# Kernel tuning notes

Measured on AMD Instinct MI355X. Metric: run time of the kernel, lower is better.

The kernel has to match this reference:

```python
import jax, jax.numpy as jnp
import numpy as np

N_NODES = 100000
N_EDGES = 600000
D = 128  # input_dim == output_dim (required by index_add into zeros_like(x) + residual)
EPS = 1e-5


def _linear_params(key, d_in, d_out):
    kw, kb = jax.random.split(key)
    bound = 1.0 / np.sqrt(d_in)
    w = jax.random.uniform(kw, (d_in, d_out), minval=-bound, maxval=bound, dtype=jnp.float32)
    b = jax.random.uniform(kb, (d_out,), minval=-bound, maxval=bound, dtype=jnp.float32)
    return w, b


def setup_inputs() -> dict:
    key = jax.random.key(0)
    ks = jax.random.split(key, 6)
    x = jax.random.normal(ks[0], (N_NODES, D), dtype=jnp.float32)
    edge_index = jax.random.randint(ks[1], (2, N_EDGES), 0, N_NODES, dtype=jnp.int32)
    w_m1, b_m1 = _linear_params(ks[2], 2 * D, D)
    w_m2, b_m2 = _linear_params(ks[3], D, D)
    w_u1, b_u1 = _linear_params(ks[4], 2 * D, D)
    w_u2, b_u2 = _linear_params(ks[5], D, D)
    gamma = jnp.ones((D,), dtype=jnp.float32)
    beta = jnp.zeros((D,), dtype=jnp.float32)
    return {
        "x": x, "edge_index": edge_index,
        "w_m1": w_m1, "b_m1": b_m1, "w_m2": w_m2, "b_m2": b_m2,
        "w_u1": w_u1, "b_u1": b_u1, "w_u2": w_u2, "b_u2": b_u2,
        "gamma": gamma, "beta": beta,
    }


def _layernorm(h, gamma, beta):
    mu = jnp.mean(h, axis=-1, keepdims=True)
    var = jnp.mean(jnp.square(h - mu), axis=-1, keepdims=True)
    return (h - mu) * jax.lax.rsqrt(var + EPS) * gamma + beta


def reference(x, edge_index, w_m1, b_m1, w_m2, b_m2, w_u1, b_u1, w_u2, b_u2, gamma, beta):
    row, col = edge_index[0], edge_index[1]
    # message MLP on concat of gathered endpoints: [E, 2D] -> [E, D]
    m_in = jnp.concatenate([x[row], x[col]], axis=-1)
    m = jax.nn.relu(m_in @ w_m1 + b_m1) @ w_m2 + b_m2
    # scatter-add messages to destination nodes (index_add along dim 0 with col)
    agg = jax.ops.segment_sum(m, col, num_segments=x.shape[0])
    # update MLP on [N, 2D] -> [N, D]
    u_in = jnp.concatenate([x, agg], axis=-1)
    h = jax.nn.relu(u_in @ w_u1 + b_u1) @ w_u2 + b_u2
    return _layernorm(h, gamma, beta) + x
```

## Files before the change

### kernel.cpp

```cpp
#include <hip/hip_runtime.h>
#include <hip/hip_bf16.h>
#include <stdint.h>

#define N_NODES 100000
#define N_EDGES 600000
#define D 128
#define EPS 1e-5f
#define SCAN_BS 512
#define ROW_MASK 0x1FFFF

#define PREP_BLOCKS 321
#define HIST_BLOCKS 2344
#define XF_BLOCKS   782

typedef __attribute__((ext_vector_type(8))) short short8;
typedef __attribute__((ext_vector_type(16))) float floatx16;


__device__ __forceinline__ uint32_t pack_bf16_rne(float lo, float hi) {
    uint32_t ul = __builtin_bit_cast(uint32_t, lo);
    uint32_t uh = __builtin_bit_cast(uint32_t, hi);
    ul += 0x7fffu + ((ul >> 16) & 1u);
    uh += 0x7fffu + ((uh >> 16) & 1u);
    return (ul >> 16) | (uh & 0xffff0000u);
}

__device__ __forceinline__ unsigned short f32_to_bf16_rne(float f) {
    uint32_t u = __builtin_bit_cast(uint32_t, f);
    u += 0x7fffu + ((u >> 16) & 1u);
    return (unsigned short)(u >> 16);
}

__device__ __forceinline__ float bflo(uint32_t a) { return __builtin_bit_cast(float, a << 16); }
__device__ __forceinline__ float bfhi(uint32_t a) { return __builtin_bit_cast(float, a & 0xffff0000u); }

__global__ void prep_hist(const float* __restrict__ w_m1, const float* __restrict__ w_u1,
                          const float* __restrict__ w_u2, const float* __restrict__ w_m2,
                          const float* __restrict__ b_m2,
                          unsigned short* __restrict__ wm1f, unsigned short* __restrict__ wu1tf,
                          unsigned short* __restrict__ wu2f, unsigned short* __restrict__ wcf,
                          float* __restrict__ vb,
                          const int* __restrict__ col, int* __restrict__ count) {
    if (blockIdx.x >= PREP_BLOCKS) {
        int e = (blockIdx.x - PREP_BLOCKS) * 256 + threadIdx.x;
        if (e < N_EDGES) atomicAdd(&count[col[e]], 1);
        return;
    }
    int idx = blockIdx.x * 256 + threadIdx.x;
    if (idx < 32768) {
        int j = idx & 7, lane = (idx >> 3) & 63, t = (idx >> 9) & 3, s = idx >> 11;
        int kk = s * 16 + ((lane >> 5) << 3) + j;
        wm1f[idx] = f32_to_bf16_rne(w_m1[kk * 128 + t * 32 + (lane & 31)]);
    } else if (idx < 49152) {
        int ii = idx - 32768;
        int j = ii & 7, lane = (ii >> 3) & 63, t = (ii >> 9) & 3, s = ii >> 11;
        int kk = s * 16 + ((lane >> 5) << 3) + j;
        wu1tf[ii] = f32_to_bf16_rne(w_u1[kk * 128 + t * 32 + (lane & 31)]);
    } else if (idx < 65536) {
        int ii = idx - 49152;
        int j = ii & 7, lane = (ii >> 3) & 63, t = (ii >> 9) & 3, s = ii >> 11;
        int kk = s * 16 + ((lane >> 5) << 3) + j;
        wu2f[ii] = f32_to_bf16_rne(w_u2[kk * 128 + t * 32 + (lane & 31)]);
    } else if (idx < 81920) {
        int ii = idx - 65536;
        int j = ii & 7, lane = (ii >> 3) & 63, t = (ii >> 9) & 3, s = ii >> 11;
        int kk = s * 16 + ((lane >> 5) << 3) + j;
        int nn = t * 32 + (lane & 31);
        float acc = 0.0f;
        for (int q = 0; q < 128; ++q)
            acc += w_m2[kk * 128 + q] * w_u1[(128 + q) * 128 + nn];
        wcf[ii] = f32_to_bf16_rne(acc);
    } else if (idx < 82048) {
        int nn = idx - 81920;
        float acc = 0.0f;
        for (int q = 0; q < 128; ++q)
            acc += b_m2[q] * w_u1[(128 + q) * 128 + nn];
        vb[nn] = acc;
    }
}

__global__ void scan_one(const int* __restrict__ count, int* __restrict__ base,
                         int* __restrict__ cursor, int* __restrict__ gcur) {
    __shared__ int tmp[SCAN_BS];
    __shared__ int bbase;
    int g = blockIdx.x * SCAN_BS + threadIdx.x;
    int v = (g < N_NODES) ? count[g] : 0;
    tmp[threadIdx.x] = v;
    __syncthreads();
    int acc = v;
#pragma unroll
    for (int off = 1; off < SCAN_BS; off <<= 1) {
        int add = (threadIdx.x >= off) ? tmp[threadIdx.x - off] : 0;
        __syncthreads();
        acc += add;
        tmp[threadIdx.x] = acc;
        __syncthreads();
    }
    if (threadIdx.x == SCAN_BS - 1) bbase = atomicAdd(gcur, acc);
    __syncthreads();
    if (g < N_NODES) {
        int b = bbase + acc - v;
        base[g] = b;
        cursor[g] = b;
    }
}

__launch_bounds__(256, 4)
__global__ void xform_scatter(const float* __restrict__ x, const short8* __restrict__ w1f,
                              const float* __restrict__ b1, unsigned short* __restrict__ xtb,
                              const int* __restrict__ row, const int* __restrict__ col,
                              int* __restrict__ cursor, int* __restrict__ srow) {
    if (blockIdx.x >= XF_BLOCKS) {
        int e = (blockIdx.x - XF_BLOCKS) * 256 + threadIdx.x;
        if (e < N_EDGES) {
            int c = col[e];
            int p = atomicAdd(&cursor[c], 1);
            srow[p] = row[e] | ((c & 31) << 17);
        }
        return;
    }

    __shared__ __align__(16) short h1[4][32 * 136];
    const int wave = threadIdx.x >> 6;
    const int lane = threadIdx.x & 63;
    const int l31  = lane & 31;
    const int half = lane >> 5;
    short* hl = h1[wave];

    const int nbase = (blockIdx.x * 4 + wave) * 32;
    const int n = min(nbase + l31, N_NODES - 1);
    const float* px = x + (size_t)n * D + half * 8;

    union { short8 v; uint32_t u[4]; } fa[8];
#pragma unroll
    for (int s = 0; s < 8; ++s) {
        const int off = s * 16;
        float4 a0 = *(const float4*)(px + off);
        float4 a1 = *(const float4*)(px + off + 4);
        fa[s].u[0] = pack_bf16_rne(a0.x, a0.y); fa[s].u[1] = pack_bf16_rne(a0.z, a0.w);
        fa[s].u[2] = pack_bf16_rne(a1.x, a1.y); fa[s].u[3] = pack_bf16_rne(a1.z, a1.w);
    }

#pragma unroll
    for (int p = 0; p < 2; ++p) {
        floatx16 acc[4];
#pragma unroll
        for (int t = 0; t < 4; ++t) acc[t] = (floatx16)0.0f;
#pragma unroll
        for (int s = 0; s < 8; ++s) {
#pragma unroll
            for (int t = 0; t < 4; ++t) {
                short8 wf = w1f[((p * 8 + s) * 4 + t) * 64 + lane];
                acc[t] = __builtin_amdgcn_mfma_f32_32x32x16_bf16(fa[s].v, wf, acc[t], 0, 0, 0);
            }
        }
#pragma unroll
        for (int t = 0; t < 4; ++t) {
            float bias = p ? b1[t * 32 + l31] : 0.0f;
#pragma unroll
            for (int r = 0; r < 16; ++r) {
                int m = (r & 3) + 8 * (r >> 2) + 4 * half;
                hl[m * 136 + t * 32 + l31] = (short)f32_to_bf16_rne(acc[t][r] + bias);
            }
        }
#pragma unroll
        for (int it = 0; it < 8; ++it) {
            int off = it * 512 + lane * 8;
            int r2 = off >> 7;
            int c2 = off & 127;
            if (nbase + r2 < N_NODES) {
                short8 v = *(const short8*)(hl + r2 * 136 + c2);
                *(short8*)(xtb + (size_t)(nbase + r2) * 256 + p * 128 + c2) = v;
            }
        }
    }
}

__launch_bounds__(256, 4)
__global__ void upd_kernel(const float* __restrict__ x, const uint32_t* __restrict__ xtb32,
                           const int* __restrict__ srowpk,
                           const int* __restrict__ base, const int* __restrict__ count,
                           const short8* __restrict__ wu1tf, const short8* __restrict__ wcf,
                           const short8* __restrict__ wu2f,
                           const float* __restrict__ b_u1, const float* __restrict__ vb,
                           const float* __restrict__ b_u2,
                           const float* __restrict__ gamma, const float* __restrict__ beta,
                           float* __restrict__ out) {
    __shared__ __align__(16) short h1[4][32 * 136];
    const int wave = threadIdx.x >> 6;
    const int lane = threadIdx.x & 63;
    const int l31  = lane & 31;
    const int half = lane >> 5;
    short* hl = h1[wave];
    uint32_t* accu = (uint32_t*)hl;

    const int nbase = (blockIdx.x * 4 + wave) * 32;
    const int nc = min(nbase + l31, N_NODES - 1);

    const int b_l = base[nc];
    const int c_l = count[nc];
    const int ebeg = __shfl(b_l, 0);
    const int eend = __shfl(b_l, 31) + __shfl(c_l, 31);
    const float dgv = (float)c_l;

#pragma unroll
    for (int i = 0; i < 32; ++i) accu[i * 64 + lane] = 0;

    {
        float s_lo = 0.0f, s_hi = 0.0f;
        int curnib = -1;
        for (int t0 = ebeg; t0 < eend; t0 += 64) {
            const int nb = min(64, eend - t0);
            int pk = (lane < nb) ? srowpk[t0 + lane] : 0;
            for (int d = 0; d < nb; d += 4) {
                int p0 = __shfl(pk, d);
                int p1 = __shfl(pk, min(d + 1, nb - 1));
                int p2 = __shfl(pk, min(d + 2, nb - 1));
                int p3 = __shfl(pk, min(d + 3, nb - 1));
                int r0 = p0 & ROW_MASK, n0 = p0 >> 17;
                int r1 = p1 & ROW_MASK, n1 = p1 >> 17;
                int r2 = p2 & ROW_MASK, n2 = p2 >> 17;
                int r3 = p3 & ROW_MASK, n3 = p3 >> 17;
                uint32_t a0 = xtb32[(size_t)r0 * 128 + lane];
                uint32_t b0 = xtb32[(size_t)(nbase + n0) * 128 + 64 + lane];
                uint32_t a1 = xtb32[(size_t)r1 * 128 + lane];
                uint32_t b1v = xtb32[(size_t)(nbase + n1) * 128 + 64 + lane];
                uint32_t a2 = xtb32[(size_t)r2 * 128 + lane];
                uint32_t b2v = xtb32[(size_t)(nbase + n2) * 128 + 64 + lane];
                uint32_t a3 = xtb32[(size_t)r3 * 128 + lane];
                uint32_t b3v = xtb32[(size_t)(nbase + n3) * 128 + 64 + lane];

                {
                    float vlo = fmaxf(bflo(a0) + bflo(b0), 0.0f);
                    float vhi = fmaxf(bfhi(a0) + bfhi(b0), 0.0f);
                    if (n0 != curnib) {
                        if (curnib >= 0) accu[curnib * 64 + lane] = pack_bf16_rne(s_lo, s_hi);
                        curnib = n0; s_lo = vlo; s_hi = vhi;
                    } else { s_lo += vlo; s_hi += vhi; }
                }
                if (d + 1 < nb) {
                    float vlo = fmaxf(bflo(a1) + bflo(b1v), 0.0f);
                    float vhi = fmaxf(bfhi(a1) + bfhi(b1v), 0.0f);
                    if (n1 != curnib) {
                        accu[curnib * 64 + lane] = pack_bf16_rne(s_lo, s_hi);
                        curnib = n1; s_lo = vlo; s_hi = vhi;
                    } else { s_lo += vlo; s_hi += vhi; }
                }
                if (d + 2 < nb) {
                    float vlo = fmaxf(bflo(a2) + bflo(b2v), 0.0f);
                    float vhi = fmaxf(bfhi(a2) + bfhi(b2v), 0.0f);
                    if (n2 != curnib) {
                        accu[curnib * 64 + lane] = pack_bf16_rne(s_lo, s_hi);
                        curnib = n2; s_lo = vlo; s_hi = vhi;
                    } else { s_lo += vlo; s_hi += vhi; }
                }
                if (d + 3 < nb) {
                    float vlo = fmaxf(bflo(a3) + bflo(b3v), 0.0f);
                    float vhi = fmaxf(bfhi(a3) + bfhi(b3v), 0.0f);
                    if (n3 != curnib) {
                        accu[curnib * 64 + lane] = pack_bf16_rne(s_lo, s_hi);
                        curnib = n3; s_lo = vlo; s_hi = vhi;
                    } else { s_lo += vlo; s_hi += vhi; }
                }
            }
        }
        if (curnib >= 0) accu[curnib * 64 + lane] = pack_bf16_rne(s_lo, s_hi);
    }

    const float* px = x + (size_t)nc * D + half * 8;

    floatx16 acc[4];
#pragma unroll
    for (int t = 0; t < 4; ++t) acc[t] = (floatx16)0.0f;

#pragma unroll
    for (int s = 0; s < 16; ++s) {
        union { short8 v; uint32_t u[4]; } fa;
        const short8* bf;
        if (s < 8) {
            const int off = s * 16;
            float4 a0 = *(const float4*)(px + off);
            float4 a1 = *(const float4*)(px + off + 4);
            fa.u[0] = pack_bf16_rne(a0.x, a0.y); fa.u[1] = pack_bf16_rne(a0.z, a0.w);
            fa.u[2] = pack_bf16_rne(a1.x, a1.y); fa.u[3] = pack_bf16_rne(a1.z, a1.w);
            bf = wu1tf + (s * 4) * 64;
        } else {
            fa.v = *(const short8*)((const short*)accu + l31 * 128 + (s - 8) * 16 + half * 8);
            bf = wcf + ((s - 8) * 4) * 64;
        }
#pragma unroll
        for (int t = 0; t < 4; ++t) {
            short8 wf = bf[t * 64 + lane];
            acc[t] = __builtin_amdgcn_mfma_f32_32x32x16_bf16(fa.v, wf, acc[t], 0, 0, 0);
        }
    }

    float bu1[4], vbt[4];
#pragma unroll
    for (int t = 0; t < 4; ++t) {
        bu1[t] = b_u1[t * 32 + l31];
        vbt[t] = vb[t * 32 + l31];
    }

#pragma unroll
    for (int r = 0; r < 16; ++r) {
        int m = (r & 3) + 8 * (r >> 2) + 4 * half;
        float dg = __shfl(dgv, m, 32);
#pragma unroll
        for (int t = 0; t < 4; ++t) {
            float v = fmaxf(acc[t][r] + bu1[t] + dg * vbt[t], 0.0f);
            hl[m * 136 + t * 32 + l31] = (short)f32_to_bf16_rne(v);
        }
    }

    floatx16 acc2[4];
#pragma unroll
    for (int t = 0; t < 4; ++t) acc2[t] = (floatx16)0.0f;

#pragma unroll
    for (int s = 0; s < 8; ++s) {
        short8 af = *(const short8*)(hl + l31 * 136 + s * 16 + half * 8);
#pragma unroll
        for (int t = 0; t < 4; ++t) {
            short8 wf = wu2f[(s * 4 + t) * 64 + lane];
            acc2[t] = __builtin_amdgcn_mfma_f32_32x32x16_bf16(af, wf, acc2[t], 0, 0, 0);
        }
    }

    float g4[4], be4[4], bias2[4];
#pragma unroll
    for (int t = 0; t < 4; ++t) {
        g4[t]    = gamma[t * 32 + l31];
        be4[t]   = beta[t * 32 + l31];
        bias2[t] = b_u2[t * 32 + l31];
    }

    float* hf = (float*)hl;
#pragma unroll
    for (int p = 0; p < 2; ++p) {
#pragma unroll
        for (int rr = 0; rr < 8; ++rr) {
            int r = p * 8 + rr;
            float hv[4];
            float s1 = 0.0f, s2 = 0.0f;
#pragma unroll
            for (int t = 0; t < 4; ++t) {
                hv[t] = acc2[t][r] + bias2[t];
                s1 += hv[t];
                s2 += hv[t] * hv[t];
            }
#pragma unroll
            for (int mask = 1; mask < 32; mask <<= 1) {
                s1 += __shfl_xor(s1, mask);
                s2 += __shfl_xor(s2, mask);
            }
            float mean = s1 * (1.0f / 128.0f);
            float var  = s2 * (1.0f / 128.0f) - mean * mean;
            float rs   = rsqrtf(var + EPS);
            int m = (r & 3) + 8 * (r >> 2) + 4 * half;
            int mrow = m - 16 * p;
#pragma unroll
            for (int t = 0; t < 4; ++t)
                hf[mrow * 132 + t * 32 + l31] = (hv[t] - mean) * rs * g4[t] + be4[t];
        }
#pragma unroll
        for (int it = 0; it < 8; ++it) {
            int q = it * 64 + lane;
            int r2 = q >> 5;
            int c4 = q & 31;
            int node = nbase + 16 * p + r2;
            if (node < N_NODES) {
                float4 v = *(const float4*)(hf + r2 * 132 + c4 * 4);
                float4 xr = *(const float4*)(x + (size_t)node * D + c4 * 4);
                v.x += xr.x; v.y += xr.y; v.z += xr.z; v.w += xr.w;
                *(float4*)(out + (size_t)node * D + c4 * 4) = v;
            }
        }
    }
}

extern "C" void kernel_launch(void* const* d_in, const int* in_sizes, int n_in,
                              void* d_out, int out_size, void* d_ws, size_t ws_size,
                              hipStream_t stream) {
    const float* x     = (const float*)d_in[0];
    const int*   edge  = (const int*)d_in[1];
    const float* w_m1  = (const float*)d_in[2];
    const float* b_m1  = (const float*)d_in[3];
    const float* w_m2  = (const float*)d_in[4];
    const float* b_m2  = (const float*)d_in[5];
    const float* w_u1  = (const float*)d_in[6];
    const float* b_u1  = (const float*)d_in[7];
    const float* w_u2  = (const float*)d_in[8];
    const float* b_u2  = (const float*)d_in[9];
    const float* gamma = (const float*)d_in[10];
    const float* beta  = (const float*)d_in[11];
    float* out = (float*)d_out;

    char* ws = (char*)d_ws;
    size_t off = 0;
    auto alloc = [&](size_t bytes) { void* p = ws + off; off = (off + bytes + 15) & ~(size_t)15; return p; };

    unsigned short* xtb   = (unsigned short*)alloc((size_t)N_NODES * 256 * 2);
    unsigned short* wm1f  = (unsigned short*)alloc(256 * 128 * 2);
    unsigned short* wu1tf = (unsigned short*)alloc(128 * 128 * 2);
    unsigned short* wcf   = (unsigned short*)alloc(128 * 128 * 2);
    unsigned short* wu2f  = (unsigned short*)alloc(128 * 128 * 2);
    float* vb    = (float*)alloc(128 * 4);
    int* count   = (int*)alloc((size_t)N_NODES * 4 + 16);
    int* gcur    = count + N_NODES;
    int* base    = (int*)alloc((size_t)N_NODES * 4);
    int* cursor  = (int*)alloc((size_t)N_NODES * 4);
    int* srow    = (int*)alloc((size_t)N_EDGES * 4);

    const int* rowi = edge;
    const int* coli = edge + N_EDGES;
    const int NB = (N_NODES + SCAN_BS - 1) / SCAN_BS;

    (void)hipMemsetAsync(count, 0, (size_t)N_NODES * 4 + 16, stream);

    prep_hist<<<PREP_BLOCKS + HIST_BLOCKS, 256, 0, stream>>>(
        w_m1, w_u1, w_u2, w_m2, b_m2, wm1f, wu1tf, wu2f, wcf, vb, coli, count);

    scan_one<<<NB, SCAN_BS, 0, stream>>>(count, base, cursor, gcur);

    xform_scatter<<<XF_BLOCKS + HIST_BLOCKS, 256, 0, stream>>>(
        x, (const short8*)wm1f, b_m1, xtb, rowi, coli, cursor, srow);

    upd_kernel<<<(N_NODES + 127) / 128, 256, 0, stream>>>(
        x, (const uint32_t*)xtb, srow, base, count,
        (const short8*)wu1tf, (const short8*)wcf, (const short8*)wu2f,
        b_u1, vb, b_u2, gamma, beta, out);
}
```

Measured before the change: 269.5 us.

## Record histogram ranks to drop scatter atomics, use one-wave blocks, widen gather batch

The histogram pass now saves each edge's atomic rank. The scatter pass computes its slot as base[col]+rank, so it no longer needs a second pass of atomics or a cursor array. The transform and update kernels are relaunched with single-wave 64-thread blocks (one 32-node tile per block), and the tail-bound guards are removed because 100000 divides evenly into 32-node tiles. The update kernel's edge gather now issues 8 loads per batch instead of 4 to raise memory-level parallelism. This costs an extra 2.4 MB rank array and more, smaller blocks.

```diff
diff --git a/kernel.cpp b/kernel.cpp
--- a/kernel.cpp
+++ b/kernel.cpp
@@ -11,7 +11,9 @@
 
 #define PREP_BLOCKS 321
 #define HIST_BLOCKS 2344
-#define XF_BLOCKS   782
+#define XF_BLOCKS   3125
+#define SC_BLOCKS   9375
+#define UPD_BLOCKS  3125
 
 typedef __attribute__((ext_vector_type(8))) short short8;
 typedef __attribute__((ext_vector_type(16))) float floatx16;
@@ -40,10 +42,11 @@
                           unsigned short* __restrict__ wm1f, unsigned short* __restrict__ wu1tf,
                           unsigned short* __restrict__ wu2f, unsigned short* __restrict__ wcf,
                           float* __restrict__ vb,
-                          const int* __restrict__ col, int* __restrict__ count) {
+                          const int* __restrict__ col, int* __restrict__ count,
+                          int* __restrict__ rank) {
     if (blockIdx.x >= PREP_BLOCKS) {
         int e = (blockIdx.x - PREP_BLOCKS) * 256 + threadIdx.x;
-        if (e < N_EDGES) atomicAdd(&count[col[e]], 1);
+        if (e < N_EDGES) rank[e] = atomicAdd(&count[col[e]], 1);
         return;
     }
     int idx = blockIdx.x * 256 + threadIdx.x;
@@ -80,7 +83,7 @@
 }
 
 __global__ void scan_one(const int* __restrict__ count, int* __restrict__ base,
-                         int* __restrict__ cursor, int* __restrict__ gcur) {
+                         int* __restrict__ gcur) {
     __shared__ int tmp[SCAN_BS];
     __shared__ int bbase;
     int g = blockIdx.x * SCAN_BS + threadIdx.x;
@@ -98,37 +101,33 @@
     }
     if (threadIdx.x == SCAN_BS - 1) bbase = atomicAdd(gcur, acc);
     __syncthreads();
-    if (g < N_NODES) {
-        int b = bbase + acc - v;
-        base[g] = b;
-        cursor[g] = b;
-    }
-}
-
-__launch_bounds__(256, 4)
+    if (g < N_NODES) base[g] = bbase + acc - v;
+}
+
+__launch_bounds__(64, 4)
 __global__ void xform_scatter(const float* __restrict__ x, const short8* __restrict__ w1f,
                               const float* __restrict__ b1, unsigned short* __restrict__ xtb,
                               const int* __restrict__ row, const int* __restrict__ col,
-                              int* __restrict__ cursor, int* __restrict__ srow) {
+                              const int* __restrict__ rank, const int* __restrict__ base,
+                              int* __restrict__ srow) {
     if (blockIdx.x >= XF_BLOCKS) {
-        int e = (blockIdx.x - XF_BLOCKS) * 256 + threadIdx.x;
+        int e = (blockIdx.x - XF_BLOCKS) * 64 + threadIdx.x;
         if (e < N_EDGES) {
             int c = col[e];
-            int p = atomicAdd(&cursor[c], 1);
+            int p = base[c] + rank[e];
             srow[p] = row[e] | ((c & 31) << 17);
         }
         return;
     }
 
-    __shared__ __align__(16) short h1[4][32 * 136];
-    const int wave = threadIdx.x >> 6;
-    const int lane = threadIdx.x & 63;
+    __shared__ __align__(16) short h1[32 * 136];
+    const int lane = threadIdx.x;
     const int l31  = lane & 31;
     const int half = lane >> 5;
-    short* hl = h1[wave];
-
-    const int nbase = (blockIdx.x * 4 + wave) * 32;
-    const int n = min(nbase + l31, N_NODES - 1);
+    short* hl = h1;
+
+    const int nbase = blockIdx.x * 32;
+    const int n = nbase + l31;
     const float* px = x + (size_t)n * D + half * 8;
 
     union { short8 v; uint32_t u[4]; } fa[8];
@@ -168,15 +167,13 @@
             int off = it * 512 + lane * 8;
             int r2 = off >> 7;
             int c2 = off & 127;
-            if (nbase + r2 < N_NODES) {
-                short8 v = *(const short8*)(hl + r2 * 136 + c2);
-                *(short8*)(xtb + (size_t)(nbase + r2) * 256 + p * 128 + c2) = v;
-            }
-        }
-    }
-}
-
-__launch_bounds__(256, 4)
+            short8 v = *(const short8*)(hl + r2 * 136 + c2);
+            *(short8*)(xtb + (size_t)(nbase + r2) * 256 + p * 128 + c2) = v;
+        }
+    }
+}
+
+__launch_bounds__(64, 4)
 __global__ void upd_kernel(const float* __restrict__ x, const uint32_t* __restrict__ xtb32,
                            const int* __restrict__ srowpk,
                            const int* __restrict__ base, const int* __restrict__ count,
@@ -186,16 +183,15 @@
                            const float* __restrict__ b_u2,
                            const float* __restrict__ gamma, const float* __restrict__ beta,
                            float* __restrict__ out) {
-    __shared__ __align__(16) short h1[4][32 * 136];
-    const int wave = threadIdx.x >> 6;
-    const int lane = threadIdx.x & 63;
+    __shared__ __align__(16) short h1[32 * 136];
+    const int lane = threadIdx.x;
     const int l31  = lane & 31;
     const int half = lane >> 5;
-    short* hl = h1[wave];
+    short* hl = h1;
     uint32_t* accu = (uint32_t*)hl;
 
-    const int nbase = (blockIdx.x * 4 + wave) * 32;
-    const int nc = min(nbase + l31, N_NODES - 1);
+    const int nbase = blockIdx.x * 32;
+    const int nc = nbase + l31;
 
     const int b_l = base[nc];
     const int c_l = count[nc];
@@ -212,55 +208,27 @@
         for (int t0 = ebeg; t0 < eend; t0 += 64) {
             const int nb = min(64, eend - t0);
             int pk = (lane < nb) ? srowpk[t0 + lane] : 0;
-            for (int d = 0; d < nb; d += 4) {
-                int p0 = __shfl(pk, d);
-                int p1 = __shfl(pk, min(d + 1, nb - 1));
-                int p2 = __shfl(pk, min(d + 2, nb - 1));
-                int p3 = __shfl(pk, min(d + 3, nb - 1));
-                int r0 = p0 & ROW_MASK, n0 = p0 >> 17;
-                int r1 = p1 & ROW_MASK, n1 = p1 >> 17;
-                int r2 = p2 & ROW_MASK, n2 = p2 >> 17;
-                int r3 = p3 & ROW_MASK, n3 = p3 >> 17;
-                uint32_t a0 = xtb32[(size_t)r0 * 128 + lane];
-                uint32_t b0 = xtb32[(size_t)(nbase + n0) * 128 + 64 + lane];
-                uint32_t a1 = xtb32[(size_t)r1 * 128 + lane];
-                uint32_t b1v = xtb32[(size_t)(nbase + n1) * 128 + 64 + lane];
-                uint32_t a2 = xtb32[(size_t)r2 * 128 + lane];
-                uint32_t b2v = xtb32[(size_t)(nbase + n2) * 128 + 64 + lane];
-                uint32_t a3 = xtb32[(size_t)r3 * 128 + lane];
-                uint32_t b3v = xtb32[(size_t)(nbase + n3) * 128 + 64 + lane];
-
-                {
-                    float vlo = fmaxf(bflo(a0) + bflo(b0), 0.0f);
-                    float vhi = fmaxf(bfhi(a0) + bfhi(b0), 0.0f);
-                    if (n0 != curnib) {
-                        if (curnib >= 0) accu[curnib * 64 + lane] = pack_bf16_rne(s_lo, s_hi);
-                        curnib = n0; s_lo = vlo; s_hi = vhi;
-                    } else { s_lo += vlo; s_hi += vhi; }
+            for (int d = 0; d < nb; d += 8) {
+                uint32_t av[8], bv[8];
+                int nn[8];
+#pragma unroll
+                for (int k = 0; k < 8; ++k) {
+                    int p = __shfl(pk, min(d + k, nb - 1));
+                    int r = p & ROW_MASK;
+                    nn[k] = p >> 17;
+                    av[k] = xtb32[(size_t)r * 128 + lane];
+                    bv[k] = xtb32[(size_t)(nbase + nn[k]) * 128 + 64 + lane];
                 }
-                if (d + 1 < nb) {
-                    float vlo = fmaxf(bflo(a1) + bflo(b1v), 0.0f);
-                    float vhi = fmaxf(bfhi(a1) + bfhi(b1v), 0.0f);
-                    if (n1 != curnib) {
-                        accu[curnib * 64 + lane] = pack_bf16_rne(s_lo, s_hi);
-                        curnib = n1; s_lo = vlo; s_hi = vhi;
-                    } else { s_lo += vlo; s_hi += vhi; }
-                }
-                if (d + 2 < nb) {
-                    float vlo = fmaxf(bflo(a2) + bflo(b2v), 0.0f);
-                    float vhi = fmaxf(bfhi(a2) + bfhi(b2v), 0.0f);
-                    if (n2 != curnib) {
-                        accu[curnib * 64 + lane] = pack_bf16_rne(s_lo, s_hi);
-                        curnib = n2; s_lo = vlo; s_hi = vhi;
-                    } else { s_lo += vlo; s_hi += vhi; }
-                }
-                if (d + 3 < nb) {
-                    float vlo = fmaxf(bflo(a3) + bflo(b3v), 0.0f);
-                    float vhi = fmaxf(bfhi(a3) + bfhi(b3v), 0.0f);
-                    if (n3 != curnib) {
-                        accu[curnib * 64 + lane] = pack_bf16_rne(s_lo, s_hi);
-                        curnib = n3; s_lo = vlo; s_hi = vhi;
-                    } else { s_lo += vlo; s_hi += vhi; }
+#pragma unroll
+                for (int k = 0; k < 8; ++k) {
+                    if (d + k < nb) {
+                        float vlo = fmaxf(bflo(av[k]) + bflo(bv[k]), 0.0f);
+                        float vhi = fmaxf(bfhi(av[k]) + bfhi(bv[k]), 0.0f);
+                        if (nn[k] != curnib) {
+                            if (curnib >= 0) accu[curnib * 64 + lane] = pack_bf16_rne(s_lo, s_hi);
+                            curnib = nn[k]; s_lo = vlo; s_hi = vhi;
+                        } else { s_lo += vlo; s_hi += vhi; }
+                    }
                 }
             }
         }
@@ -369,12 +337,10 @@
             int r2 = q >> 5;
             int c4 = q & 31;
             int node = nbase + 16 * p + r2;
-            if (node < N_NODES) {
-                float4 v = *(const float4*)(hf + r2 * 132 + c4 * 4);
-                float4 xr = *(const float4*)(x + (size_t)node * D + c4 * 4);
-                v.x += xr.x; v.y += xr.y; v.z += xr.z; v.w += xr.w;
-                *(float4*)(out + (size_t)node * D + c4 * 4) = v;
-            }
+            float4 v = *(const float4*)(hf + r2 * 132 + c4 * 4);
+            float4 xr = *(const float4*)(x + (size_t)node * D + c4 * 4);
+            v.x += xr.x; v.y += xr.y; v.z += xr.z; v.w += xr.w;
+            *(float4*)(out + (size_t)node * D + c4 * 4) = v;
         }
     }
 }
@@ -409,7 +375,7 @@
     int* count   = (int*)alloc((size_t)N_NODES * 4 + 16);
     int* gcur    = count + N_NODES;
     int* base    = (int*)alloc((size_t)N_NODES * 4);
-    int* cursor  = (int*)alloc((size_t)N_NODES * 4);
+    int* rank    = (int*)alloc((size_t)N_EDGES * 4);
     int* srow    = (int*)alloc((size_t)N_EDGES * 4);
 
     const int* rowi = edge;
@@ -419,14 +385,14 @@
     (void)hipMemsetAsync(count, 0, (size_t)N_NODES * 4 + 16, stream);
 
     prep_hist<<<PREP_BLOCKS + HIST_BLOCKS, 256, 0, stream>>>(
-        w_m1, w_u1, w_u2, w_m2, b_m2, wm1f, wu1tf, wu2f, wcf, vb, coli, count);
-
-    scan_one<<<NB, SCAN_BS, 0, stream>>>(count, base, cursor, gcur);
-
-    xform_scatter<<<XF_BLOCKS + HIST_BLOCKS, 256, 0, stream>>>(
-        x, (const short8*)wm1f, b_m1, xtb, rowi, coli, cursor, srow);
-
-    upd_kernel<<<(N_NODES + 127) / 128, 256, 0, stream>>>(
+        w_m1, w_u1, w_u2, w_m2, b_m2, wm1f, wu1tf, wu2f, wcf, vb, coli, count, rank);
+
+    scan_one<<<NB, SCAN_BS, 0, stream>>>(count, base, gcur);
+
+    xform_scatter<<<XF_BLOCKS + SC_BLOCKS, 64, 0, stream>>>(
+        x, (const short8*)wm1f, b_m1, xtb, rowi, coli, rank, base, srow);
+
+    upd_kernel<<<UPD_BLOCKS, 64, 0, stream>>>(
         x, (const uint32_t*)xtb, srow, base, count,
         (const short8*)wu1tf, (const short8*)wcf, (const short8*)wu2f,
         b_u1, vb, b_u2, gamma, beta, out);
```

Measured after the change: 258.3 us. 1.04x faster.
